# Performance work log

Measured on AMD Instinct MI355X. Metric: run time of the kernel, lower is better.

The kernel has to match this reference:

```python
import jax, jax.numpy as jnp
import numpy as np

TOP_K = 2


def setup_inputs() -> dict:
    key = jax.random.key(0)
    k1, k2 = jax.random.split(key)
    x = jax.random.normal(k1, (4, 4096, 2048), dtype=jnp.float32)
    # router weight, init std=0.01 as in the module
    w_router = jax.random.normal(k2, (64, 2048), dtype=jnp.float32) * 0.01
    return {"x": x, "w_router": w_router}


def reference(x, w_router):
    B, S, D = x.shape
    E = w_router.shape[0]
    N = B * S  # num_tokens
    xt = x.reshape(N, D)
    # router linear (no bias, no jitter: eval mode / jitter=0)
    router_logits = jnp.einsum("nd,ed->ne", xt, w_router)  # [N, E]
    router_probs = jax.nn.softmax(router_logits, axis=-1)
    top_k_probs, top_k_indices = jax.lax.top_k(router_probs, TOP_K)  # [N, K]
    top_k_probs_norm = top_k_probs / jnp.sum(top_k_probs, axis=-1, keepdims=True)
    # load-balancing aux loss
    router_prob_per_expert = jnp.mean(router_probs, axis=0)  # [E]
    aux_loss = jnp.mean(E * router_prob_per_expert * router_prob_per_expert)
    # vectorized scatter replacing the python double-loop:
    # dispatch[token, expert] = normalized top-k prob
    token_idx = jnp.arange(N)[:, None]  # [N, 1] broadcasts over K
    dispatch_tensor = jnp.zeros((N, E), dtype=x.dtype).at[token_idx, top_k_indices].set(top_k_probs_norm)
    combine_tensor = dispatch_tensor
    return (dispatch_tensor, combine_tensor, router_logits, router_probs,
            aux_loss, top_k_indices, top_k_probs_norm)
```

## Files before the change

### kernel.cpp

```cpp
#include <hip/hip_runtime.h>

#define D_DIM 2048
#define E_DIM 64
#define BT 256
#define DSPLIT 4
#define DCH (D_DIM / DSPLIT)
#define DK 16
#define NTILE (DCH / DK)
#define XB (BT * DK * 4)
#define WB (E_DIM * DK * 4)
#define BUFB (XB + WB)
#define NBUF 4

typedef __attribute__((address_space(3))) char as3_char;
typedef __attribute__((address_space(1))) const char as1_char;

__global__ __launch_bounds__(256, 1) void router_gemm(
    const float* __restrict__ x, const float* __restrict__ w,
    float* __restrict__ out, int N) {
  __shared__ __align__(16) char lds[NBUF][BUFB];
  const int tid = threadIdx.x;
  const int l = tid & 63;
  const int wv = tid >> 6;
  const int tbase = blockIdx.x * BT;
  const int dbase = blockIdx.y * DCH;

  const int scol = ((l & 3) ^ ((l >> 3) & 3)) * 4;
  const float* xsrc[4];
#pragma unroll
  for (int q = 0; q < 4; ++q) {
    int row = (wv * 4 + q) * 16 + (l >> 2);
    xsrc[q] = x + (size_t)(tbase + row) * D_DIM + dbase + scol;
  }
  const float* wsrc = w + (size_t)(wv * 16 + (l >> 2)) * D_DIM + dbase + scol;

  auto STAGE = [&](int b, int t) {
    const int d0 = t * DK;
#pragma unroll
    for (int q = 0; q < 4; ++q)
      __builtin_amdgcn_global_load_lds((as1_char*)(const char*)(xsrc[q] + d0),
                                       (as3_char*)&lds[b][(wv * 4 + q) * 1024],
                                       16, 0, 0);
    __builtin_amdgcn_global_load_lds((as1_char*)(const char*)(wsrc + d0),
                                     (as3_char*)&lds[b][XB + wv * 1024], 16, 0, 0);
  };

  const int tg = tid & 31;
  const int eg = tid >> 5;
  int xoff[8], woff[8];
#pragma unroll
  for (int i = 0; i < 8; ++i)
    xoff[i] = (tg + 32 * i) * 64 + (((tg >> 1) & 3) << 4);
#pragma unroll
  for (int j = 0; j < 8; ++j) {
    int e = eg * 8 + j;
    woff[j] = XB + e * 64 + (((e >> 1) & 3) << 4);
  }

  float acc[8][8];
#pragma unroll
  for (int i = 0; i < 8; ++i)
#pragma unroll
    for (int j = 0; j < 8; ++j) acc[i][j] = 0.f;

  STAGE(0, 0);
  STAGE(1, 1);
  STAGE(2, 2);

  for (int t = 0; t < NTILE; ++t) {
    if (t + 2 < NTILE) {
      asm volatile("s_waitcnt vmcnt(10)" ::: "memory");
    } else if (t + 2 == NTILE) {
      asm volatile("s_waitcnt vmcnt(5)" ::: "memory");
    } else {
      asm volatile("s_waitcnt vmcnt(0)" ::: "memory");
    }
    __builtin_amdgcn_s_barrier();
    __builtin_amdgcn_sched_barrier(0);
    if (t + 3 < NTILE) STAGE((t + 3) & 3, t + 3);

    const char* buf = lds[t & 3];
#pragma unroll
    for (int d4 = 0; d4 < 4; ++d4) {
      const int dx = d4 << 4;
      float4 xv[8], wvv[8];
#pragma unroll
      for (int i = 0; i < 8; ++i)
        xv[i] = *(const float4*)(buf + (xoff[i] ^ dx));
#pragma unroll
      for (int j = 0; j < 8; ++j)
        wvv[j] = *(const float4*)(buf + (woff[j] ^ dx));
#pragma unroll
      for (int i = 0; i < 8; ++i)
#pragma unroll
        for (int j = 0; j < 8; ++j) {
          acc[i][j] = fmaf(xv[i].x, wvv[j].x, acc[i][j]);
          acc[i][j] = fmaf(xv[i].y, wvv[j].y, acc[i][j]);
          acc[i][j] = fmaf(xv[i].z, wvv[j].z, acc[i][j]);
          acc[i][j] = fmaf(xv[i].w, wvv[j].w, acc[i][j]);
        }
    }
  }

  float* part = out + (size_t)blockIdx.y * ((size_t)N * E_DIM);
#pragma unroll
  for (int i = 0; i < 8; ++i) {
    size_t o = (size_t)(tbase + tg + 32 * i) * E_DIM + eg * 8;
    *(float4*)(part + o) = make_float4(acc[i][0], acc[i][1], acc[i][2], acc[i][3]);
    *(float4*)(part + o + 4) = make_float4(acc[i][4], acc[i][5], acc[i][6], acc[i][7]);
  }
}

__global__ __launch_bounds__(256) void postprocess(float* out, float* ws, int N) {
  const int lane = threadIdx.x & 63;
  const int wv = threadIdx.x >> 6;
  const size_t NE = (size_t)N * E_DIM;
  float* disp = out;
  float* comb = out + NE;
  float* logits_o = out + 2 * NE;
  float* probs_o = out + 3 * NE;
  float* idx_o = out + 4 * NE + 1;
  float* pn_o = out + 4 * NE + 1 + 2 * (size_t)N;

  float expsum = 0.f;
  const int t0 = blockIdx.x * 64 + wv * 16;
  for (int k = 0; k < 16; ++k) {
    const size_t t = (size_t)(t0 + k);
    const size_t o = t * E_DIM + lane;
    float lv = (disp[o] + comb[o]) + (logits_o[o] + probs_o[o]);
    logits_o[o] = lv;
    float m = lv;
#pragma unroll
    for (int off = 32; off; off >>= 1) m = fmaxf(m, __shfl_xor(m, off));
    float p = __expf(lv - m);
    float s = p;
#pragma unroll
    for (int off = 32; off; off >>= 1) s += __shfl_xor(s, off);
    float prob = p / s;
    probs_o[o] = prob;
    expsum += prob;

    unsigned long long key =
        ((unsigned long long)__float_as_uint(prob) << 32) | (unsigned)(63 - lane);
    unsigned long long k1 = key;
#pragma unroll
    for (int off = 32; off; off >>= 1) {
      unsigned long long v = __shfl_xor(k1, off);
      if (v > k1) k1 = v;
    }
    int i1 = 63 - (int)(k1 & 63);
    unsigned long long k2 = (lane == i1) ? 0ull : key;
#pragma unroll
    for (int off = 32; off; off >>= 1) {
      unsigned long long v = __shfl_xor(k2, off);
      if (v > k2) k2 = v;
    }
    int i2 = 63 - (int)(k2 & 63);
    float p1 = __uint_as_float((unsigned)(k1 >> 32));
    float p2 = __uint_as_float((unsigned)(k2 >> 32));
    float inv = 1.0f / (p1 + p2);
    float pn1 = p1 * inv, pn2 = p2 * inv;
    float dval = (lane == i1) ? pn1 : ((lane == i2) ? pn2 : 0.f);
    disp[o] = dval;
    comb[o] = dval;
    if (lane == 0) {
      idx_o[2 * t] = (float)i1;
      idx_o[2 * t + 1] = (float)i2;
      pn_o[2 * t] = pn1;
      pn_o[2 * t + 1] = pn2;
    }
  }

  __shared__ float aux_s[4][64];
  aux_s[wv][lane] = expsum;
  __syncthreads();
  if (threadIdx.x < 64) {
    float s = aux_s[0][threadIdx.x] + aux_s[1][threadIdx.x] +
              aux_s[2][threadIdx.x] + aux_s[3][threadIdx.x];
    ws[(size_t)blockIdx.x * 64 + threadIdx.x] = s;
  }
}

__global__ __launch_bounds__(256) void finalize_aux(const float* __restrict__ ws,
                                                    float* __restrict__ auxp,
                                                    int nblocks, int N) {
  __shared__ float red[256];
  const int e = threadIdx.x & 63;
  const int part = threadIdx.x >> 6;
  float s = 0.f;
  for (int b = part; b < nblocks; b += 4) s += ws[(size_t)b * 64 + e];
  red[threadIdx.x] = s;
  __syncthreads();
  if (threadIdx.x < 64) {
    float tot = red[e] + red[64 + e] + red[128 + e] + red[192 + e];
    float pb = tot / (float)N;
    float v = pb * pb;
#pragma unroll
    for (int off = 32; off; off >>= 1) v += __shfl_xor(v, off);
    if (threadIdx.x == 0) *auxp = v;
  }
}

extern "C" void kernel_launch(void* const* d_in, const int* in_sizes, int n_in,
                              void* d_out, int out_size, void* d_ws, size_t ws_size,
                              hipStream_t stream) {
  (void)n_in; (void)out_size; (void)ws_size;
  const float* x = (const float*)d_in[0];
  const float* w = (const float*)d_in[1];
  float* out = (float*)d_out;
  const int N = in_sizes[0] / D_DIM;
  const int npb = N / 64;

  dim3 gg(N / BT, DSPLIT);
  router_gemm<<<gg, dim3(256), 0, stream>>>(x, w, out, N);
  postprocess<<<dim3(npb), dim3(256), 0, stream>>>(out, (float*)d_ws, N);
  finalize_aux<<<dim3(1), dim3(256), 0, stream>>>((const float*)d_ws,
                                                  out + 4 * (size_t)N * E_DIM,
                                                  npb, N);
}
```

Measured before the change: 288.3 us.

## Stream router weights from global into registers and halve token tile

Router weights no longer pass through LDS. Each thread loads its 8 expert rows straight from global memory into registers, double-buffered across half-tiles, and LDS now holds only x tiles. The token tile drops from 256 to 128 and launch bounds allow 2 blocks per CU, which shrinks the accumulator array and aims to raise occupancy and cut LDS traffic. In exchange the weights are re-read from cache on every tile. The single fixed vmcnt(16) wait may also over-wait and shorten the effective prefetch depth.

New measurement: 293.5 us. No clear change (+1.8%).

```diff
diff --git a/kernel.cpp b/kernel.cpp
--- a/kernel.cpp
+++ b/kernel.cpp
@@ -2,23 +2,21 @@
 
 #define D_DIM 2048
 #define E_DIM 64
-#define BT 256
+#define BT 128
 #define DSPLIT 4
 #define DCH (D_DIM / DSPLIT)
 #define DK 16
 #define NTILE (DCH / DK)
 #define XB (BT * DK * 4)
-#define WB (E_DIM * DK * 4)
-#define BUFB (XB + WB)
 #define NBUF 4
 
 typedef __attribute__((address_space(3))) char as3_char;
 typedef __attribute__((address_space(1))) const char as1_char;
 
-__global__ __launch_bounds__(256, 1) void router_gemm(
+__global__ __launch_bounds__(256, 2) void router_gemm(
     const float* __restrict__ x, const float* __restrict__ w,
     float* __restrict__ out, int N) {
-  __shared__ __align__(16) char lds[NBUF][BUFB];
+  __shared__ __align__(16) char lds[NBUF][XB];
   const int tid = threadIdx.x;
   const int l = tid & 63;
   const int wv = tid >> 6;
@@ -26,85 +24,111 @@
   const int dbase = blockIdx.y * DCH;
 
   const int scol = ((l & 3) ^ ((l >> 3) & 3)) * 4;
-  const float* xsrc[4];
-#pragma unroll
-  for (int q = 0; q < 4; ++q) {
-    int row = (wv * 4 + q) * 16 + (l >> 2);
+  const float* xsrc[2];
+#pragma unroll
+  for (int q = 0; q < 2; ++q) {
+    int row = (wv * 2 + q) * 16 + (l >> 2);
     xsrc[q] = x + (size_t)(tbase + row) * D_DIM + dbase + scol;
   }
-  const float* wsrc = w + (size_t)(wv * 16 + (l >> 2)) * D_DIM + dbase + scol;
 
   auto STAGE = [&](int b, int t) {
     const int d0 = t * DK;
 #pragma unroll
-    for (int q = 0; q < 4; ++q)
-      __builtin_amdgcn_global_load_lds((as1_char*)(const char*)(xsrc[q] + d0),
-                                       (as3_char*)&lds[b][(wv * 4 + q) * 1024],
-                                       16, 0, 0);
-    __builtin_amdgcn_global_load_lds((as1_char*)(const char*)(wsrc + d0),
-                                     (as3_char*)&lds[b][XB + wv * 1024], 16, 0, 0);
+    for (int q = 0; q < 2; ++q)
+      __builtin_amdgcn_global_load_lds(
+          (as1_char*)(const char*)(xsrc[q] + d0),
+          (as3_char*)&lds[b][(wv * 2 + q) * 1024], 16, 0, 0);
   };
 
   const int tg = tid & 31;
   const int eg = tid >> 5;
-  int xoff[8], woff[8];
-#pragma unroll
-  for (int i = 0; i < 8; ++i)
+  int xoff[4];
+#pragma unroll
+  for (int i = 0; i < 4; ++i)
     xoff[i] = (tg + 32 * i) * 64 + (((tg >> 1) & 3) << 4);
-#pragma unroll
-  for (int j = 0; j < 8; ++j) {
-    int e = eg * 8 + j;
-    woff[j] = XB + e * 64 + (((e >> 1) & 3) << 4);
-  }
-
-  float acc[8][8];
-#pragma unroll
-  for (int i = 0; i < 8; ++i)
+
+  const float* wp[8];
+#pragma unroll
+  for (int j = 0; j < 8; ++j)
+    wp[j] = w + (size_t)(eg * 8 + j) * D_DIM + dbase;
+
+  float acc[4][8];
+#pragma unroll
+  for (int i = 0; i < 4; ++i)
 #pragma unroll
     for (int j = 0; j < 8; ++j) acc[i][j] = 0.f;
+
+  float4 wAv[8][2], wBv[8][2];
 
   STAGE(0, 0);
   STAGE(1, 1);
   STAGE(2, 2);
+#pragma unroll
+  for (int j = 0; j < 8; ++j)
+#pragma unroll
+    for (int p = 0; p < 2; ++p)
+      wAv[j][p] = *(const float4*)(wp[j] + p * 4);
 
   for (int t = 0; t < NTILE; ++t) {
-    if (t + 2 < NTILE) {
-      asm volatile("s_waitcnt vmcnt(10)" ::: "memory");
-    } else if (t + 2 == NTILE) {
-      asm volatile("s_waitcnt vmcnt(5)" ::: "memory");
-    } else {
-      asm volatile("s_waitcnt vmcnt(0)" ::: "memory");
-    }
+    asm volatile("s_waitcnt vmcnt(16)" ::: "memory");
     __builtin_amdgcn_s_barrier();
     __builtin_amdgcn_sched_barrier(0);
+
+#pragma unroll
+    for (int j = 0; j < 8; ++j)
+#pragma unroll
+      for (int p = 0; p < 2; ++p)
+        wBv[j][p] = *(const float4*)(wp[j] + t * DK + 8 + p * 4);
     if (t + 3 < NTILE) STAGE((t + 3) & 3, t + 3);
 
     const char* buf = lds[t & 3];
-#pragma unroll
-    for (int d4 = 0; d4 < 4; ++d4) {
-      const int dx = d4 << 4;
-      float4 xv[8], wvv[8];
-#pragma unroll
-      for (int i = 0; i < 8; ++i)
-        xv[i] = *(const float4*)(buf + (xoff[i] ^ dx));
+
+#pragma unroll
+    for (int c = 0; c < 2; ++c) {
+      float4 xv[4];
+#pragma unroll
+      for (int i = 0; i < 4; ++i)
+        xv[i] = *(const float4*)(buf + (xoff[i] ^ (c << 4)));
+#pragma unroll
+      for (int i = 0; i < 4; ++i)
+#pragma unroll
+        for (int j = 0; j < 8; ++j) {
+          acc[i][j] = fmaf(xv[i].x, wAv[j][c].x, acc[i][j]);
+          acc[i][j] = fmaf(xv[i].y, wAv[j][c].y, acc[i][j]);
+          acc[i][j] = fmaf(xv[i].z, wAv[j][c].z, acc[i][j]);
+          acc[i][j] = fmaf(xv[i].w, wAv[j][c].w, acc[i][j]);
+        }
+    }
+
+    if (t + 1 < NTILE) {
 #pragma unroll
       for (int j = 0; j < 8; ++j)
-        wvv[j] = *(const float4*)(buf + (woff[j] ^ dx));
-#pragma unroll
-      for (int i = 0; i < 8; ++i)
+#pragma unroll
+        for (int p = 0; p < 2; ++p)
+          wAv[j][p] = *(const float4*)(wp[j] + (t + 1) * DK + p * 4);
+    }
+
+#pragma unroll
+    for (int c = 0; c < 2; ++c) {
+      float4 xv[4];
+#pragma unroll
+      for (int i = 0; i < 4; ++i)
+        xv[i] = *(const float4*)(buf + (xoff[i] ^ ((c + 2) << 4)));
+#pragma unroll
+      for (int i = 0; i < 4; ++i)
 #pragma unroll
         for (int j = 0; j < 8; ++j) {
-          acc[i][j] = fmaf(xv[i].x, wvv[j].x, acc[i][j]);
-          acc[i][j] = fmaf(xv[i].y, wvv[j].y, acc[i][j]);
-          acc[i][j] = fmaf(xv[i].z, wvv[j].z, acc[i][j]);
-          acc[i][j] = fmaf(xv[i].w, wvv[j].w, acc[i][j]);
+          acc[i][j] = fmaf(xv[i].x, wBv[j][c].x, acc[i][j]);
+          acc[i][j] = fmaf(xv[i].y, wBv[j][c].y, acc[i][j]);
+          acc[i][j] = fmaf(xv[i].z, wBv[j][c].z, acc[i][j]);
+          acc[i][j] = fmaf(xv[i].w, wBv[j][c].w, acc[i][j]);
         }
     }
   }
 
   float* part = out + (size_t)blockIdx.y * ((size_t)N * E_DIM);
 #pragma unroll
-  for (int i = 0; i < 8; ++i) {
+  for (int i = 0; i < 4; ++i) {
     size_t o = (size_t)(tbase + tg + 32 * i) * E_DIM + eg * 8;
     *(float4*)(part + o) = make_float4(acc[i][0], acc[i][1], acc[i][2], acc[i][3]);
     *(float4*)(part + o + 4) = make_float4(acc[i][4], acc[i][5], acc[i][6], acc[i][7]);
```
